# Kernel optimization log

Hardware: AMD Instinct MI355X
Metric: run time of the kernel (lower is better)

## Reference

```python
import jax, jax.numpy as jnp
import numpy as np

S, B, TD = 1024, 2, 138
D, H, Dh, L, F = 1024, 16, 64, 8, 2048
EPS = 1e-5


def setup_inputs() -> dict:
    key = jax.random.key(0)
    ks = jax.random.split(key, 32)
    std = 0.02

    def w(k, shape):
        return (jax.random.normal(k, shape, jnp.float32) * std)

    return {
        'tokens': jax.random.normal(ks[0], (S, B, TD), jnp.float32),
        'Win': w(ks[1], (D, TD)), 'bin_': jnp.zeros((D,), jnp.float32),
        'pos_emb': w(ks[2], (S, D)),
        'Wq': w(ks[3], (L, D, D)), 'bq': jnp.zeros((L, D), jnp.float32),
        'Wk': w(ks[4], (L, D, D)), 'bk': jnp.zeros((L, D), jnp.float32),
        'Wv': w(ks[5], (L, D, D)), 'bv': jnp.zeros((L, D), jnp.float32),
        'Wo': w(ks[6], (L, D, D)), 'bo': jnp.zeros((L, D), jnp.float32),
        'W1': w(ks[7], (L, F, D)), 'b1': jnp.zeros((L, F), jnp.float32),
        'W2': w(ks[8], (L, D, F)), 'b2': jnp.zeros((L, D), jnp.float32),
        'g1': jnp.ones((L, D), jnp.float32), 'be1': jnp.zeros((L, D), jnp.float32),
        'g2': jnp.ones((L, D), jnp.float32), 'be2': jnp.zeros((L, D), jnp.float32),
        'Wh': w(ks[9], (1, D)), 'bh': jnp.zeros((1,), jnp.float32),
    }


def _ln(x, g, b):
    mu = jnp.mean(x, axis=-1, keepdims=True)
    var = jnp.mean(jnp.square(x - mu), axis=-1, keepdims=True)
    return (x - mu) * jax.lax.rsqrt(var + EPS) * g + b


def _rope_tables(seq_len):
    inv_freq = 1.0 / (10000.0 ** (jnp.arange(0, Dh, 2, dtype=jnp.float32) / Dh))
    ang = jnp.arange(seq_len, dtype=jnp.float32)[:, None] * inv_freq  # (S, Dh/2)
    cos = jnp.repeat(jnp.cos(ang), 2, axis=-1)  # (S, Dh) interleaved
    sin = jnp.repeat(jnp.sin(ang), 2, axis=-1)
    return cos, sin


def _apply_rope(x, cos, sin):
    # x: (B, H, S, Dh); rotate_every_two: pairs (x0, x1) -> (-x1, x0)
    rot = jnp.stack([-x[..., 1::2], x[..., 0::2]], axis=-1).reshape(x.shape)
    return x * cos + rot * sin


def reference(tokens, Win, bin_, pos_emb, Wq, bq, Wk, bk, Wv, bv, Wo, bo,
              W1, b1, W2, b2, g1, be1, g2, be2, Wh, bh):
    s = tokens.shape[0]
    x = jnp.einsum('sbt,dt->sbd', tokens, Win) + bin_ + pos_emb[:s, None, :]
    cos, sin = _rope_tables(s)
    causal = jnp.tril(jnp.ones((s, s), dtype=bool))
    scale = 1.0 / np.sqrt(Dh)

    def to_heads(y):  # (S,B,D) -> (B,H,S,Dh)
        return jnp.transpose(y.reshape(s, -1, H, Dh), (1, 2, 0, 3))

    def layer(x, p):
        wq, bq_, wk, bk_, wv, bv_, wo, bo_, w1, b1_, w2, b2_, g1_, be1_, g2_, be2_ = p
        qh = _apply_rope(to_heads(jnp.einsum('sbd,ed->sbe', x, wq) + bq_), cos, sin)
        kh = _apply_rope(to_heads(jnp.einsum('sbd,ed->sbe', x, wk) + bk_), cos, sin)
        vh = to_heads(jnp.einsum('sbd,ed->sbe', x, wv) + bv_)
        scores = jnp.einsum('bhqd,bhkd->bhqk', qh, kh) * scale
        scores = jnp.where(causal, scores, -jnp.inf)
        attn = jax.nn.softmax(scores, axis=-1)
        o = jnp.einsum('bhqk,bhkd->bhqd', attn, vh)  # (B,H,S,Dh)
        o = jnp.transpose(o, (2, 0, 1, 3)).reshape(s, -1, D)
        attn_out = jnp.einsum('sbd,ed->sbe', o, wo) + bo_
        src2 = _ln(x + attn_out, g1_, be1_)
        ff = jnp.einsum('sbf,df->sbd', jax.nn.relu(jnp.einsum('sbd,fd->sbf', src2, w1) + b1_), w2) + b2_
        return _ln(src2 + ff, g2_, be2_), None

    params = (Wq, bq, Wk, bk, Wv, bv, Wo, bo, W1, b1, W2, b2, g1, be1, g2, be2)
    x, _ = jax.lax.scan(layer, x, params)
    return jnp.einsum('sbd,od->sbo', x, Wh) + bh  # (S, B, 1)
```

## Files before the change

### kernel.cpp

```cpp
#include <hip/hip_runtime.h>
#include <hip/hip_bf16.h>

typedef __hip_bfloat16 bf16;
typedef float f32x4 __attribute__((ext_vector_type(4)));
typedef float f32x16 __attribute__((ext_vector_type(16)));
typedef short s16x8 __attribute__((ext_vector_type(8)));
typedef int i32x4 __attribute__((ext_vector_type(4)));

#define S_LEN 1024
#define BATCH 2
#define TDIM 138
#define KPAD 192
#define DMOD 1024
#define NHEAD 16
#define DHEAD 64
#define NLAYER 8
#define FDIM 2048
#define MROWS 2048
static const size_t DD_ = (size_t)DMOD * DMOD;
static const size_t FD_ = (size_t)FDIM * DMOD;
static const size_t LW_ = 4 * DD_ + 2 * FD_;

__device__ __forceinline__ void load_lds16(const bf16* g, bf16* l) {
  __builtin_amdgcn_global_load_lds((const __attribute__((address_space(1))) void*)g,
                                   (__attribute__((address_space(3))) void*)l, 16, 0, 0);
}

__device__ __forceinline__ unsigned pack2(float a, float b) {
  unsigned x = __builtin_bit_cast(unsigned short, __float2bfloat16(a));
  unsigned y = __builtin_bit_cast(unsigned short, __float2bfloat16(b));
  return x | (y << 16);
}

__device__ __forceinline__ int chunk_start(int c) {
  return c == 0 ? 0 : (c == 1 ? 32 : (c == 2 ? 56 : 72));
}

__global__ __launch_bounds__(256) void f2b_all(
    const float4* __restrict__ Wq, const float4* __restrict__ Wk,
    const float4* __restrict__ Wv, const float4* __restrict__ Wo,
    const float4* __restrict__ W1, const float4* __restrict__ W2,
    ushort4* __restrict__ dst, int nlay) {
  const int DD4 = (int)(DD_ / 4), FD4 = (int)(FD_ / 4), LW4 = 4 * DD4 + 2 * FD4;
  int total = nlay * LW4;
  for (int i = blockIdx.x * 256 + threadIdx.x; i < total; i += gridDim.x * 256) {
    int l = i / LW4, off = i - l * LW4;
    const float4* src; int o2;
    if (off < 3 * DD4) {
      int w = off / DD4; o2 = off - w * DD4 + l * DD4;
      src = w == 0 ? Wq : (w == 1 ? Wk : Wv);
    } else if (off < 4 * DD4) { src = Wo; o2 = off - 3 * DD4 + l * DD4; }
    else if (off < 4 * DD4 + FD4) { src = W1; o2 = off - 4 * DD4 + l * FD4; }
    else { src = W2; o2 = off - 4 * DD4 - FD4 + l * FD4; }
    float4 v = src[o2];
    ushort4 o;
    o.x = __builtin_bit_cast(unsigned short, __float2bfloat16(v.x));
    o.y = __builtin_bit_cast(unsigned short, __float2bfloat16(v.y));
    o.z = __builtin_bit_cast(unsigned short, __float2bfloat16(v.z));
    o.w = __builtin_bit_cast(unsigned short, __float2bfloat16(v.w));
    dst[i] = o;
  }
}

__global__ __launch_bounds__(256) void pad_cvt(const float* __restrict__ in,
                                               bf16* __restrict__ out, int R) {
  int i = blockIdx.x * 256 + threadIdx.x;
  if (i >= R * KPAD) return;
  int r = i / KPAD, t = i - r * KPAD;
  out[i] = __float2bfloat16(t < TDIM ? in[r * TDIM + t] : 0.0f);
}

__global__ __launch_bounds__(256) void rope_table(float2* __restrict__ t) {
  int idx = blockIdx.x * 256 + threadIdx.x;
  if (idx >= S_LEN * 32) return;
  int s = idx >> 5, i = idx & 31;
  float freq = __expf(-(float)i * (2.0f / (float)DHEAD) * 9.210340371976184f);
  float sn, cs;
  sincosf((float)s * freq, &sn, &cs);
  t[idx] = make_float2(cs, sn);
}

template<int EPI, int SPLITK>
__global__ __launch_bounds__(256) void gemm64(
    const bf16* __restrict__ A, const bf16* __restrict__ W,
    const float* __restrict__ b0p, const float* __restrict__ b1p, const float* __restrict__ b2p,
    const float2* __restrict__ rope2, float* __restrict__ Cf,
    bf16* __restrict__ Cb0, bf16* __restrict__ Cb1, bf16* __restrict__ Cb2,
    int N, int K, int nby) {
  constexpr int ASZ = 64 * 64, BSZ = 128 * 64;
  __shared__ bf16 As[2 * ASZ];
  __shared__ bf16 Bs[2 * BSZ];
  int nwg = gridDim.x, bid = blockIdx.x;
  int wg = (bid & 7) * (nwg >> 3) + (bid >> 3);
  int nbx = N >> 7;
  int by = wg % nby, bx2 = wg / nby;
  int kh = 0, bx = bx2;
  if constexpr (SPLITK == 2) { bx = bx2 % nbx; kh = bx2 / nbx; }
  int bn = bx * 128, bm = by * 64;
  int Kh = K / SPLITK, koff = kh * Kh;
  int tid = threadIdx.x, lane = tid & 63, w = tid >> 6;
  int lo = lane & 15, hi = lane >> 4;
  int wr = (w >> 1) * 32, wc = (w & 1) * 64;
  f32x4 acc[2][4] = {};

  int srow = tid >> 3;
  int scol = (tid & 7) * 8;
  int scolsw = scol ^ ((srow & 7) << 3);
  const bf16* gA = A + (size_t)(bm + srow) * K + koff + scolsw;
  const bf16* gB = W + (size_t)(bn + srow) * K + koff + scolsw;
  bf16* lA = As + srow * 64 + scol;
  bf16* lB = Bs + srow * 64 + scol;

  auto STAGE = [&](int k0, int b) {
    load_lds16(gA + k0, lA + b * ASZ);
    load_lds16(gA + (size_t)32 * K + k0, lA + b * ASZ + 32 * 64);
    load_lds16(gB + k0, lB + b * BSZ);
    load_lds16(gB + (size_t)32 * K + k0, lB + b * BSZ + 32 * 64);
    load_lds16(gB + (size_t)64 * K + k0, lB + b * BSZ + 64 * 64);
    load_lds16(gB + (size_t)96 * K + k0, lB + b * BSZ + 96 * 64);
  };

  int nt = Kh / 64;
  STAGE(0, 0);
  __syncthreads();
  int cur = 0;
  int rsw = (lo & 7) << 3;
  for (int t = 0; t < nt; t++) {
    if (t + 1 < nt) STAGE((t + 1) * 64, cur ^ 1);
    const bf16* Ab = As + cur * ASZ;
    const bf16* Bb = Bs + cur * BSZ;
#pragma unroll
    for (int ks = 0; ks < 2; ks++) {
      int col = ((ks * 32 + hi * 8) ^ rsw);
      s16x8 af[2], bfr[4];
#pragma unroll
      for (int mi = 0; mi < 2; mi++) af[mi] = *(const s16x8*)(Ab + (wr + mi * 16 + lo) * 64 + col);
#pragma unroll
      for (int nj = 0; nj < 4; nj++) bfr[nj] = *(const s16x8*)(Bb + (wc + nj * 16 + lo) * 64 + col);
#pragma unroll
      for (int mi = 0; mi < 2; mi++)
#pragma unroll
        for (int nj = 0; nj < 4; nj++)
          acc[mi][nj] = __builtin_amdgcn_mfma_f32_16x16x32_bf16(af[mi], bfr[nj], acc[mi][nj], 0, 0, 0);
    }
    __syncthreads();
    cur ^= 1;
  }

#pragma unroll
  for (int mi = 0; mi < 2; mi++)
#pragma unroll
    for (int nj = 0; nj < 4; nj++)
#pragma unroll
      for (int r = 0; r < 4; r++) {
        int m = bm + wr + mi * 16 + hi * 4 + r;
        int n = bn + wc + nj * 16 + lo;
        float v = acc[mi][nj][r];
        if constexpr (EPI == 0) {
          int which = n >> 10;
          int d = n & 1023, h = d >> 6, dh = d & 63;
          int s = m >> 1, bb = m & 1;
          const float* bp = which == 0 ? b0p : (which == 1 ? b1p : b2p);
          v += bp[d];
          if (which < 2) {
            float pv = __shfl_xor(v, 1);
            float2 cn = rope2[s * 32 + (dh >> 1)];
            float o = (dh & 1) ? (v * cn.x + pv * cn.y) : (v * cn.x - pv * cn.y);
            bf16* dst = which == 0 ? Cb0 : Cb1;
            dst[(((size_t)(bb * NHEAD + h)) * S_LEN + s) * DHEAD + dh] = __float2bfloat16(o);
          } else {
            Cb2[(((size_t)(bb * NHEAD + h)) * DHEAD + dh) * S_LEN + s] = __float2bfloat16(v);
          }
        } else if constexpr (EPI == 1) {
          if (SPLITK == 1 || kh == 0) v += b0p[n];
          Cf[((size_t)kh * MROWS + m) * N + n] = v;
        } else if constexpr (EPI == 2) {
          Cb0[(size_t)m * N + n] = __float2bfloat16(fmaxf(v + b0p[n], 0.0f));
        } else {
          float v2 = v + b0p[n] + b1p[(size_t)(m >> 1) * DMOD + n];
          Cf[(size_t)m * N + n] = v2;
          Cb0[(size_t)m * N + n] = __float2bfloat16(v2);
        }
      }
}

__global__ __launch_bounds__(256) void flash_part(const bf16* __restrict__ Q,
    const bf16* __restrict__ K, const bf16* __restrict__ Vt,
    float* __restrict__ pO, float* __restrict__ pML) {
  int bid = blockIdx.x;
  int xcd = bid & 7, idx = bid >> 3;
  int bh = xcd * 4 + idx / 20;
  int w = threadIdx.x >> 6, lane = threadIdx.x & 63;
  int widx = (idx % 20) * 4 + w;
  int c = widx < 32 ? 0 : (widx < 56 ? 1 : (widx < 72 ? 2 : 3));
  int qt = widx - chunk_start(c) + 8 * c;
  int l31 = lane & 31, hi1 = lane >> 5;
  int q0 = qt * 32, kc0 = c * 256;
  int kend = min(kc0 + 256, q0 + 32);
  int nkt = (kend - kc0 + 31) >> 5;

  const size_t qkb = (size_t)bh * S_LEN * DHEAD;
  const bf16* qp = Q + qkb + (size_t)(q0 + l31) * DHEAD + hi1 * 8;
  s16x8 bq0 = *(const s16x8*)(qp);
  s16x8 bq1 = *(const s16x8*)(qp + 16);
  s16x8 bq2 = *(const s16x8*)(qp + 32);
  s16x8 bq3 = *(const s16x8*)(qp + 48);
  const bf16* kB = K + qkb;
  const bf16* vB = Vt + qkb;
  f32x16 accO0 = {}, accO1 = {};
  float mv = -INFINITY, lv = 0.0f;
  const float SC = 0.18033688011112042f;

  auto loadTile = [&](int kc, s16x8& k0, s16x8& k1, s16x8& k2, s16x8& k3,
                      s16x8& v0, s16x8& v1, s16x8& v2, s16x8& v3) {
    const bf16* kp = kB + (size_t)(kc + l31) * DHEAD + hi1 * 8;
    k0 = *(const s16x8*)(kp);
    k1 = *(const s16x8*)(kp + 16);
    k2 = *(const s16x8*)(kp + 32);
    k3 = *(const s16x8*)(kp + 48);
    const bf16* vp = vB + (size_t)l31 * S_LEN + kc + hi1 * 8;
    v0 = *(const s16x8*)(vp);
    v1 = *(const s16x8*)(vp + 16);
    v2 = *(const s16x8*)(vp + (size_t)32 * S_LEN);
    v3 = *(const s16x8*)(vp + (size_t)32 * S_LEN + 16);
  };

  auto computeTile = [&](int kc, s16x8 ka0, s16x8 ka1, s16x8 ka2, s16x8 ka3,
                         s16x8 va00, s16x8 va01, s16x8 va10, s16x8 va11) {
    f32x16 st = {};
    st = __builtin_amdgcn_mfma_f32_32x32x16_bf16(ka0, bq0, st, 0, 0, 0);
    st = __builtin_amdgcn_mfma_f32_32x32x16_bf16(ka1, bq1, st, 0, 0, 0);
    st = __builtin_amdgcn_mfma_f32_32x32x16_bf16(ka2, bq2, st, 0, 0, 0);
    st = __builtin_amdgcn_mfma_f32_32x32x16_bf16(ka3, bq3, st, 0, 0, 0);

    bool diag = (kc >= q0);
    float pmax = -INFINITY;
#pragma unroll
    for (int j = 0; j < 16; j++) {
      float s = st[j] * SC;
      if (diag) {
        int krow = kc + (j & 3) + 8 * (j >> 2) + 4 * hi1;
        if (krow > q0 + l31) s = -INFINITY;
      }
      st[j] = s;
      pmax = fmaxf(pmax, s);
    }
    pmax = fmaxf(pmax, __shfl_xor(pmax, 32));
    float mnew = fmaxf(mv, pmax);
    float fs = exp2f(mv - mnew);
    float sum = 0.0f;
#pragma unroll
    for (int j = 0; j < 16; j++) {
      float e = exp2f(st[j] - mnew);
      st[j] = e;
      sum += e;
    }
    sum += __shfl_xor(sum, 32);
    lv = lv * fs + sum;
    mv = mnew;
    accO0 = accO0 * fs;
    accO1 = accO1 * fs;

    unsigned w0 = pack2(st[0], st[1]),   w1 = pack2(st[2], st[3]);
    unsigned w2 = pack2(st[4], st[5]),   w3 = pack2(st[6], st[7]);
    unsigned w4 = pack2(st[8], st[9]),   w5 = pack2(st[10], st[11]);
    unsigned w6 = pack2(st[12], st[13]), w7 = pack2(st[14], st[15]);
    unsigned xw0 = (unsigned)__shfl_xor((int)w0, 32), xw1 = (unsigned)__shfl_xor((int)w1, 32);
    unsigned xw2 = (unsigned)__shfl_xor((int)w2, 32), xw3 = (unsigned)__shfl_xor((int)w3, 32);
    unsigned xw4 = (unsigned)__shfl_xor((int)w4, 32), xw5 = (unsigned)__shfl_xor((int)w5, 32);
    unsigned xw6 = (unsigned)__shfl_xor((int)w6, 32), xw7 = (unsigned)__shfl_xor((int)w7, 32);
    bool hb = (hi1 != 0);
    i32x4 f0, f1;
    f0.x = (int)(hb ? xw2 : w0); f0.y = (int)(hb ? xw3 : w1);
    f0.z = (int)(hb ? w2 : xw0); f0.w = (int)(hb ? w3 : xw1);
    f1.x = (int)(hb ? xw6 : w4); f1.y = (int)(hb ? xw7 : w5);
    f1.z = (int)(hb ? w6 : xw4); f1.w = (int)(hb ? w7 : xw5);
    s16x8 pf0 = __builtin_bit_cast(s16x8, f0);
    s16x8 pf1 = __builtin_bit_cast(s16x8, f1);
    accO0 = __builtin_amdgcn_mfma_f32_32x32x16_bf16(va00, pf0, accO0, 0, 0, 0);
    accO0 = __builtin_amdgcn_mfma_f32_32x32x16_bf16(va01, pf1, accO0, 0, 0, 0);
    accO1 = __builtin_amdgcn_mfma_f32_32x32x16_bf16(va10, pf0, accO1, 0, 0, 0);
    accO1 = __builtin_amdgcn_mfma_f32_32x32x16_bf16(va11, pf1, accO1, 0, 0, 0);
  };

  s16x8 A0, A1, A2, A3, A4, A5, A6, A7;
  s16x8 B0, B1, B2, B3, B4, B5, B6, B7;
  loadTile(kc0, A0, A1, A2, A3, A4, A5, A6, A7);
  for (int kt = 0; kt < nkt; kt += 2) {
    if (kt + 1 < nkt) loadTile(kc0 + (kt + 1) * 32, B0, B1, B2, B3, B4, B5, B6, B7);
    computeTile(kc0 + kt * 32, A0, A1, A2, A3, A4, A5, A6, A7);
    if (kt + 1 < nkt) {
      if (kt + 2 < nkt) loadTile(kc0 + (kt + 2) * 32, A0, A1, A2, A3, A4, A5, A6, A7);
      computeTile(kc0 + (kt + 1) * 32, B0, B1, B2, B3, B4, B5, B6, B7);
    }
  }

  int pbase = bh * 80 + widx;
  float* po = pO + (size_t)pbase * 2048 + l31 * 64 + 4 * hi1;
#pragma unroll
  for (int jj = 0; jj < 4; jj++) {
    f32x4 v0 = {accO0[4 * jj], accO0[4 * jj + 1], accO0[4 * jj + 2], accO0[4 * jj + 3]};
    f32x4 v1 = {accO1[4 * jj], accO1[4 * jj + 1], accO1[4 * jj + 2], accO1[4 * jj + 3]};
    *(f32x4*)(po + 8 * jj) = v0;
    *(f32x4*)(po + 32 + 8 * jj) = v1;
  }
  if (hi1 == 0) {
    pML[pbase * 64 + l31] = mv;
    pML[pbase * 64 + 32 + l31] = lv;
  }
}

__global__ __launch_bounds__(256) void flash_merge(const float* __restrict__ pO,
    const float* __restrict__ pML, bf16* __restrict__ O) {
  int bid = blockIdx.x;
  int xcd = bid & 7, idx = bid >> 3;
  int bh = xcd * 4 + idx / 32, qt = idx % 32;
  int b = bh >> 4, h = bh & 15;
  int nch = (qt >> 3) + 1;
  int t = threadIdx.x;
  int dh = t & 63, r0 = t >> 6;
  int ibase = bh * 80;
#pragma unroll
  for (int j = 0; j < 8; j++) {
    int row = j * 4 + r0;
    float ms = -INFINITY;
    for (int cc = 0; cc < nch; cc++) {
      int wi = chunk_start(cc) + qt - 8 * cc;
      ms = fmaxf(ms, pML[(ibase + wi) * 64 + row]);
    }
    float l = 0.0f, o = 0.0f;
    for (int cc = 0; cc < nch; cc++) {
      int wi = chunk_start(cc) + qt - 8 * cc;
      float wgt = exp2f(pML[(ibase + wi) * 64 + row] - ms);
      l += wgt * pML[(ibase + wi) * 64 + 32 + row];
      o += wgt * pO[(size_t)(ibase + wi) * 2048 + row * 64 + dh];
    }
    int q = qt * 32 + row;
    O[((size_t)q * BATCH + b) * DMOD + h * DHEAD + dh] = __float2bfloat16(o / l);
  }
}

__global__ __launch_bounds__(256) void ln_kernel(const float* __restrict__ a,
    const float* __restrict__ r0, const float* __restrict__ r1,
    const float* __restrict__ g, const float* __restrict__ be,
    float* __restrict__ outf, bf16* __restrict__ outb) {
  int m = blockIdx.x;
  int tid = threadIdx.x;
  float vals[4];
  float s1 = 0.f, s2 = 0.f;
  for (int j = 0; j < 4; j++) {
    int d = tid + j * 256;
    size_t i = (size_t)m * DMOD + d;
    float v = a[i] + r0[i] + r1[i];
    vals[j] = v; s1 += v; s2 += v * v;
  }
  __shared__ float red[8];
  for (int d = 1; d < 64; d <<= 1) { s1 += __shfl_xor(s1, d); s2 += __shfl_xor(s2, d); }
  int w = tid >> 6, lane = tid & 63;
  if (lane == 0) { red[w] = s1; red[4 + w] = s2; }
  __syncthreads();
  s1 = red[0] + red[1] + red[2] + red[3];
  s2 = red[4] + red[5] + red[6] + red[7];
  float mean = s1 * (1.0f / DMOD);
  float var = s2 * (1.0f / DMOD) - mean * mean;
  float rstd = rsqrtf(var + 1e-5f);
  for (int j = 0; j < 4; j++) {
    int d = tid + j * 256;
    float o = (vals[j] - mean) * rstd * g[d] + be[d];
    outf[(size_t)m * DMOD + d] = o;
    outb[(size_t)m * DMOD + d] = __float2bfloat16(o);
  }
}

__global__ __launch_bounds__(256) void head_kernel(const float* __restrict__ x,
    const float* __restrict__ Wh, const float* __restrict__ bh, float* __restrict__ out) {
  int m = blockIdx.x * 4 + (threadIdx.x >> 6);
  int lane = threadIdx.x & 63;
  float s = 0.f;
  for (int j = 0; j < 16; j++) {
    int d = lane + j * 64;
    s += x[(size_t)m * DMOD + d] * Wh[d];
  }
  for (int d = 1; d < 64; d <<= 1) s += __shfl_xor(s, d);
  if (lane == 0) out[m] = s + bh[0];
}

extern "C" void kernel_launch(void* const* d_in, const int* in_sizes, int n_in,
                              void* d_out, int out_size, void* d_ws, size_t ws_size,
                              hipStream_t stream) {
  (void)in_sizes; (void)n_in; (void)out_size;
  const float* tokens = (const float*)d_in[0];
  const float* Win    = (const float*)d_in[1];
  const float* binp   = (const float*)d_in[2];
  const float* pos    = (const float*)d_in[3];
  const float* Wq     = (const float*)d_in[4];
  const float* bq     = (const float*)d_in[5];
  const float* Wk     = (const float*)d_in[6];
  const float* bk     = (const float*)d_in[7];
  const float* Wv     = (const float*)d_in[8];
  const float* bv     = (const float*)d_in[9];
  const float* Wo     = (const float*)d_in[10];
  const float* bo     = (const float*)d_in[11];
  const float* W1     = (const float*)d_in[12];
  const float* b1     = (const float*)d_in[13];
  const float* W2     = (const float*)d_in[14];
  const float* b2     = (const float*)d_in[15];
  const float* g1     = (const float*)d_in[16];
  const float* be1    = (const float*)d_in[17];
  const float* g2     = (const float*)d_in[18];
  const float* be2    = (const float*)d_in[19];
  const float* Wh     = (const float*)d_in[20];
  const float* bhp    = (const float*)d_in[21];
  float* out = (float*)d_out;

  char* p = (char*)d_ws;
  auto alloc = [&](size_t bytes) { char* r = p; p += (bytes + 255) & ~(size_t)255; return r; };
  float* xf   = (float*)alloc((size_t)MROWS * DMOD * 4);
  bf16*  xb   = (bf16*) alloc((size_t)MROWS * DMOD * 2);
  float* x2f  = (float*)alloc((size_t)MROWS * DMOD * 4);
  bf16*  x2b  = (bf16*) alloc((size_t)MROWS * DMOD * 2);
  float* tmpf = (float*)alloc((size_t)2 * MROWS * DMOD * 4);
  bf16*  qb   = (bf16*) alloc((size_t)MROWS * DMOD * 2);
  bf16*  kb   = (bf16*) alloc((size_t)MROWS * DMOD * 2);
  bf16*  vt   = (bf16*) alloc((size_t)MROWS * DMOD * 2);
  bf16*  ob   = (bf16*) alloc((size_t)MROWS * DMOD * 2);
  bf16*  hb   = (bf16*) alloc((size_t)MROWS * FDIM * 2);
  bf16*  tokb = (bf16*) alloc((size_t)MROWS * KPAD * 2);
  bf16*  winb = (bf16*) alloc((size_t)DMOD * KPAD * 2);
  float2* rope2 = (float2*)alloc((size_t)S_LEN * 32 * 8);
  float* pO   = (float*)alloc((size_t)32 * 80 * 2048 * 4);
  float* pML  = (float*)alloc((size_t)32 * 80 * 64 * 4);

  size_t used = (size_t)(p - (char*)d_ws);
  bool big = (ws_size - used) >= (size_t)NLAYER * LW_ * 2 + 1024;
  int nlayConv = big ? NLAYER : 1;
  bf16* wb = (bf16*)alloc((size_t)nlayConv * LW_ * 2);

  rope_table<<<(S_LEN * 32 + 255) / 256, 256, 0, stream>>>(rope2);
  pad_cvt<<<(MROWS * KPAD + 255) / 256, 256, 0, stream>>>(tokens, tokb, MROWS);
  pad_cvt<<<(DMOD * KPAD + 255) / 256, 256, 0, stream>>>(Win, winb, DMOD);
  if (big)
    f2b_all<<<2048, 256, 0, stream>>>(
        (const float4*)Wq, (const float4*)Wk, (const float4*)Wv,
        (const float4*)Wo, (const float4*)W1, (const float4*)W2,
        (ushort4*)wb, NLAYER);

  gemm64<3, 1><<<256, 256, 0, stream>>>(
      tokb, winb, binp, pos, nullptr, nullptr,
      xf, xb, nullptr, nullptr, DMOD, KPAD, 32);

  for (int l = 0; l < NLAYER; l++) {
    if (!big)
      f2b_all<<<2048, 256, 0, stream>>>(
          (const float4*)(Wq + l * DD_), (const float4*)(Wk + l * DD_),
          (const float4*)(Wv + l * DD_), (const float4*)(Wo + l * DD_),
          (const float4*)(W1 + l * FD_), (const float4*)(W2 + l * FD_),
          (ushort4*)wb, 1);
    bf16* wbl = big ? wb + (size_t)l * LW_ : wb;

    gemm64<0, 1><<<768, 256, 0, stream>>>(
        xb, wbl, bq + l * DMOD, bk + l * DMOD, bv + l * DMOD, rope2,
        nullptr, qb, kb, vt, 3 * DMOD, DMOD, 32);

    flash_part<<<640, 256, 0, stream>>>(qb, kb, vt, pO, pML);
    flash_merge<<<1024, 256, 0, stream>>>(pO, pML, ob);

    gemm64<1, 2><<<512, 256, 0, stream>>>(
        ob, wbl + 3 * DD_, bo + l * DMOD, nullptr, nullptr, nullptr,
        tmpf, nullptr, nullptr, nullptr, DMOD, DMOD, 32);

    ln_kernel<<<MROWS, 256, 0, stream>>>(xf, tmpf, tmpf + (size_t)MROWS * DMOD,
                                         g1 + l * DMOD, be1 + l * DMOD, x2f, x2b);

    gemm64<2, 1><<<512, 256, 0, stream>>>(
        x2b, wbl + 4 * DD_, b1 + l * FDIM, nullptr, nullptr, nullptr,
        nullptr, hb, nullptr, nullptr, FDIM, DMOD, 32);

    gemm64<1, 2><<<512, 256, 0, stream>>>(
        hb, wbl + 4 * DD_ + FD_, b2 + l * DMOD, nullptr, nullptr, nullptr,
        tmpf, nullptr, nullptr, nullptr, DMOD, FDIM, 32);

    ln_kernel<<<MROWS, 256, 0, stream>>>(x2f, tmpf, tmpf + (size_t)MROWS * DMOD,
                                         g2 + l * DMOD, be2 + l * DMOD, xf, xb);
  }

  head_kernel<<<MROWS / 4, 256, 0, stream>>>(xf, Wh, bhp, out);
}
```

Measured before the change: 1.452 ms.

## Store attention partials in bf16, finalize single-chunk tiles directly, remap GEMM blocks

Flash partial outputs are now stored as bf16 instead of fp32, which halves partial-buffer traffic. The first 8 query tiles need only one key chunk, so they normalize and write final output directly, and the merge kernel launches only for the remaining tiles. The GEMM block-to-tile mapping is changed to group 8 row-blocks per XCD chunk, aiming for better L2 reuse. Rounding partial outputs to bf16 before merging adds some precision loss.

```diff
diff --git a/kernel.cpp b/kernel.cpp
--- a/kernel.cpp
+++ b/kernel.cpp
@@ -6,6 +6,7 @@
 typedef float f32x16 __attribute__((ext_vector_type(16)));
 typedef short s16x8 __attribute__((ext_vector_type(8)));
 typedef int i32x4 __attribute__((ext_vector_type(4)));
+typedef unsigned u32x2 __attribute__((ext_vector_type(2)));
 
 #define S_LEN 1024
 #define BATCH 2
@@ -17,6 +18,7 @@
 #define NLAYER 8
 #define FDIM 2048
 #define MROWS 2048
+#define NITEM 80
 static const size_t DD_ = (size_t)DMOD * DMOD;
 static const size_t FD_ = (size_t)FDIM * DMOD;
 static const size_t LW_ = 4 * DD_ + 2 * FD_;
@@ -91,9 +93,15 @@
   __shared__ bf16 As[2 * ASZ];
   __shared__ bf16 Bs[2 * BSZ];
   int nwg = gridDim.x, bid = blockIdx.x;
-  int wg = (bid & 7) * (nwg >> 3) + (bid >> 3);
+  int x = bid & 7, c = bid >> 3;
+  int chunkSz = nwg >> 3;
+  int bxc = chunkSz / nby;
+  int per = 8 * bxc;
+  int grp = c / per, r0_ = c - grp * per;
+  int bxl = r0_ >> 3, byg = r0_ & 7;
+  int by = grp * 8 + byg;
+  int bx2 = x * bxc + bxl;
   int nbx = N >> 7;
-  int by = wg % nby, bx2 = wg / nby;
   int kh = 0, bx = bx2;
   if constexpr (SPLITK == 2) { bx = bx2 % nbx; kh = bx2 / nbx; }
   int bn = bx * 128, bm = by * 64;
@@ -186,7 +194,7 @@
 
 __global__ __launch_bounds__(256) void flash_part(const bf16* __restrict__ Q,
     const bf16* __restrict__ K, const bf16* __restrict__ Vt,
-    float* __restrict__ pO, float* __restrict__ pML) {
+    bf16* __restrict__ pO, float* __restrict__ pML, bf16* __restrict__ O) {
   int bid = blockIdx.x;
   int xcd = bid & 7, idx = bid >> 3;
   int bh = xcd * 4 + idx / 20;
@@ -295,31 +303,50 @@
     }
   }
 
-  int pbase = bh * 80 + widx;
-  float* po = pO + (size_t)pbase * 2048 + l31 * 64 + 4 * hi1;
-#pragma unroll
-  for (int jj = 0; jj < 4; jj++) {
-    f32x4 v0 = {accO0[4 * jj], accO0[4 * jj + 1], accO0[4 * jj + 2], accO0[4 * jj + 3]};
-    f32x4 v1 = {accO1[4 * jj], accO1[4 * jj + 1], accO1[4 * jj + 2], accO1[4 * jj + 3]};
-    *(f32x4*)(po + 8 * jj) = v0;
-    *(f32x4*)(po + 32 + 8 * jj) = v1;
-  }
-  if (hi1 == 0) {
-    pML[pbase * 64 + l31] = mv;
-    pML[pbase * 64 + 32 + l31] = lv;
-  }
-}
-
-__global__ __launch_bounds__(256) void flash_merge(const float* __restrict__ pO,
+  if (widx < 8) {
+    int b = bh >> 4, h = bh & 15;
+    float linv = 1.0f / lv;
+    bf16* po = O + ((size_t)(q0 + l31) * BATCH + b) * DMOD + h * DHEAD + 4 * hi1;
+#pragma unroll
+    for (int jj = 0; jj < 4; jj++) {
+      u32x2 v0, v1;
+      v0.x = pack2(accO0[4 * jj] * linv, accO0[4 * jj + 1] * linv);
+      v0.y = pack2(accO0[4 * jj + 2] * linv, accO0[4 * jj + 3] * linv);
+      v1.x = pack2(accO1[4 * jj] * linv, accO1[4 * jj + 1] * linv);
+      v1.y = pack2(accO1[4 * jj + 2] * linv, accO1[4 * jj + 3] * linv);
+      *(u32x2*)(po + 8 * jj) = v0;
+      *(u32x2*)(po + 32 + 8 * jj) = v1;
+    }
+  } else {
+    int pbase = bh * NITEM + widx;
+    bf16* po = pO + (size_t)pbase * 2048 + l31 * 64 + 4 * hi1;
+#pragma unroll
+    for (int jj = 0; jj < 4; jj++) {
+      u32x2 v0, v1;
+      v0.x = pack2(accO0[4 * jj], accO0[4 * jj + 1]);
+      v0.y = pack2(accO0[4 * jj + 2], accO0[4 * jj + 3]);
+      v1.x = pack2(accO1[4 * jj], accO1[4 * jj + 1]);
+      v1.y = pack2(accO1[4 * jj + 2], accO1[4 * jj + 3]);
+      *(u32x2*)(po + 8 * jj) = v0;
+      *(u32x2*)(po + 32 + 8 * jj) = v1;
+    }
+    if (hi1 == 0) {
+      pML[pbase * 64 + l31] = mv;
+      pML[pbase * 64 + 32 + l31] = lv;
+    }
+  }
+}
+
+__global__ __launch_bounds__(256) void flash_merge(const bf16* __restrict__ pO,
     const float* __restrict__ pML, bf16* __restrict__ O) {
   int bid = blockIdx.x;
   int xcd = bid & 7, idx = bid >> 3;
-  int bh = xcd * 4 + idx / 32, qt = idx % 32;
+  int bh = xcd * 4 + idx / 24, qt = idx % 24 + 8;
   int b = bh >> 4, h = bh & 15;
   int nch = (qt >> 3) + 1;
   int t = threadIdx.x;
   int dh = t & 63, r0 = t >> 6;
-  int ibase = bh * 80;
+  int ibase = bh * NITEM;
 #pragma unroll
   for (int j = 0; j < 8; j++) {
     int row = j * 4 + r0;
@@ -333,7 +360,7 @@
       int wi = chunk_start(cc) + qt - 8 * cc;
       float wgt = exp2f(pML[(ibase + wi) * 64 + row] - ms);
       l += wgt * pML[(ibase + wi) * 64 + 32 + row];
-      o += wgt * pO[(size_t)(ibase + wi) * 2048 + row * 64 + dh];
+      o += wgt * __bfloat162float(pO[(size_t)(ibase + wi) * 2048 + row * 64 + dh]);
     }
     int q = qt * 32 + row;
     O[((size_t)q * BATCH + b) * DMOD + h * DHEAD + dh] = __float2bfloat16(o / l);
@@ -428,8 +455,8 @@
   bf16*  tokb = (bf16*) alloc((size_t)MROWS * KPAD * 2);
   bf16*  winb = (bf16*) alloc((size_t)DMOD * KPAD * 2);
   float2* rope2 = (float2*)alloc((size_t)S_LEN * 32 * 8);
-  float* pO   = (float*)alloc((size_t)32 * 80 * 2048 * 4);
-  float* pML  = (float*)alloc((size_t)32 * 80 * 64 * 4);
+  bf16*  pO   = (bf16*) alloc((size_t)32 * NITEM * 2048 * 2);
+  float* pML  = (float*)alloc((size_t)32 * NITEM * 64 * 4);
 
   size_t used = (size_t)(p - (char*)d_ws);
   bool big = (ws_size - used) >= (size_t)NLAYER * LW_ * 2 + 1024;
@@ -462,8 +489,8 @@
         xb, wbl, bq + l * DMOD, bk + l * DMOD, bv + l * DMOD, rope2,
         nullptr, qb, kb, vt, 3 * DMOD, DMOD, 32);
 
-    flash_part<<<640, 256, 0, stream>>>(qb, kb, vt, pO, pML);
-    flash_merge<<<1024, 256, 0, stream>>>(pO, pML, ob);
+    flash_part<<<640, 256, 0, stream>>>(qb, kb, vt, pO, pML, ob);
+    flash_merge<<<768, 256, 0, stream>>>(pO, pML, ob);
 
     gemm64<1, 2><<<512, 256, 0, stream>>>(
         ob, wbl + 3 * DD_, bo + l * DMOD, nullptr, nullptr, nullptr,
```

After: 1.380 ms. 4.9% less time.
